# Kernel optimization log

Hardware: AMD Instinct MI355X
Metric: run time of the kernel (lower is better)

The kernel has to match this reference:

```python
import jax, jax.numpy as jnp
import numpy as np

B = 4096
L = 15          # self.length
NINP = 256      # emb_size
NHID = 512      # hidden_size
VOCAB = 30005
TOPK = 10
K = 4 * TOPK + 2   # 42 actions
N_SPLIT = 2 * TOPK
N_STEP = 5      # num_edits
PAD = 30003


def _lstm_dir(x, Wih, Whh, b, reverse):
    # x: [T,B,D]; Wih: [4H,D]; Whh: [4H,H]; b: [4H] (b_ih+b_hh). PyTorch gate order i,f,g,o.
    Bsz, H = x.shape[1], Whh.shape[1]
    def step(carry, xt):
        h, c = carry
        z = xt @ Wih.T + h @ Whh.T + b
        i, f, g, o = jnp.split(z, 4, axis=-1)
        c = jax.nn.sigmoid(f) * c + jax.nn.sigmoid(i) * jnp.tanh(g)
        h = jax.nn.sigmoid(o) * jnp.tanh(c)
        return (h, c), h
    h0 = jnp.zeros((Bsz, H), x.dtype)
    _, ys = jax.lax.scan(step, (h0, h0), x, reverse=reverse)
    return ys  # [T,B,H], position-aligned for both directions


def bilstm(x, Wih0, Whh0, b0, Wih1, Whh1, b1):
    # x: [B,T,D] -> [B,T,2H]; 2-layer bidirectional, zero initial state (matches c0/h0 zeros).
    xt = jnp.swapaxes(x, 0, 1)
    for Wih, Whh, b in ((Wih0, Whh0, b0), (Wih1, Whh1, b1)):
        fw = _lstm_dir(xt, Wih[0], Whh[0], b[0], False)
        bw = _lstm_dir(xt, Wih[1], Whh[1], b[1], True)
        xt = jnp.concatenate([fw, bw], axis=-1)
    return jnp.swapaxes(xt, 0, 1)


def policy_step(st_1, length_t, pos, emb0, key_pos, rep_words, valid_id,
                emb_table, enc_table, Wih0, Whh0, b0, Wih1, Whh1, b1,
                del_vec, hold_vec, mlp_W, mlp_b, mlp1_W, mlp1_b):
    Bsz = st_1.shape[0]
    pos_row = jnp.zeros((L,), jnp.float32).at[pos].set(1.0)         # static pos
    pos_tensor = jnp.broadcast_to(pos_row[None, :, None], (Bsz, L, 1))
    embt = emb_table[st_1] * (1.0 - pos_tensor)
    x = jnp.concatenate([embt, emb0, pos_tensor], axis=2)            # [B,L,2*ninp+1]
    out = bilstm(x, Wih0, Whh0, b0, Wih1, Whh1, b1)                  # [B,L,2*nhid]
    pooled = out[:, pos, :]
    representation = jnp.concatenate(
        [pooled, key_pos[:, pos:pos + 1], jnp.broadcast_to(pos_row[None, :], (Bsz, L))], axis=1)
    # external encoder output is detached in the original
    word_emb = jax.lax.stop_gradient(enc_table[rep_words])           # [B,4*topk,ninp]
    emb2 = jnp.concatenate([word_emb,
                            jnp.broadcast_to(del_vec, (Bsz, 1, NINP)),
                            jnp.broadcast_to(hold_vec, (Bsz, 1, NINP))], axis=1)  # [B,K,ninp]
    onehot = jnp.broadcast_to(jnp.eye(K, dtype=jnp.float32)[None], (Bsz, K, K))
    emb2 = jnp.concatenate([emb2, onehot], axis=2)                   # [B,K,ninp+K]
    rep100 = representation @ mlp_W.T + mlp_b                        # [B,100]
    emb100 = emb2 @ mlp1_W.T + mlp1_b                                # [B,K,100]
    score = jnp.einsum('bkd,bd->bk', emb100, rep100)
    policy = jax.nn.softmax(score, axis=1)
    action = jnp.argmax(policy, axis=1, keepdims=True).astype(jnp.int32)  # eval mode
    pi = jnp.take_along_axis(policy, action, axis=1)                 # [B,1]

    rep_b = (action < N_SPLIT).astype(jnp.int32)
    replaceflag = rep_b * valid_id
    ins_b = ((action >= N_SPLIT) & (action < 2 * N_SPLIT)).astype(jnp.int32)
    insertflag = ins_b * valid_id * (length_t + ins_b <= 15).astype(jnp.int32)
    del_b = (action == 2 * N_SPLIT).astype(jnp.int32)
    deleteflag = del_b * valid_id * (length_t - del_b > 2).astype(jnp.int32)
    holdflag = 1 - replaceflag - insertflag - deleteflag

    action_words = jnp.take_along_axis(rep_words, jnp.clip(action, 0, N_SPLIT - 1), axis=1)  # [B,1]
    rep_seq = jnp.concatenate([action_words, st_1[:, pos + 1:]], axis=1)
    ins_seq = jnp.concatenate([action_words, st_1[:, pos:-1]], axis=1)
    padding = jnp.full((Bsz, 1), PAD, dtype=st_1.dtype)
    del_seq = jnp.concatenate([st_1[:, pos + 1:], padding], axis=1)
    hol_seq = st_1[:, pos:]
    new_tail = (rep_seq * replaceflag + ins_seq * insertflag
                + del_seq * deleteflag + hol_seq * holdflag)
    st = st_1.at[:, pos:].set(new_tail)
    length_tt = insertflag + length_t - deleteflag
    return st, pi, action.astype(jnp.float32), length_tt


def setup_inputs() -> dict:
    key = jax.random.key(0)
    ks = jax.random.split(key, 20)
    s = 0.05
    in0 = 2 * NINP + 1
    in1 = 2 * NHID
    inp = {
        'input_ids': jax.random.randint(ks[0], (B, L), 0, 30000, dtype=jnp.int32),
        'key_pos': jax.random.uniform(ks[1], (B, L), dtype=jnp.float32),
        'sequence_length': jax.random.randint(ks[2], (B, 1), 3, 16, dtype=jnp.int32),
        'rep_words_all': jax.random.randint(ks[3], (B, N_STEP, 4 * TOPK), 0, 30000, dtype=jnp.int32),
        'valid_id_all': jax.random.randint(ks[4], (B, N_STEP, 1), 0, 2, dtype=jnp.int32),
        'emb_table': jax.random.normal(ks[5], (VOCAB, NINP), jnp.float32) * s,
        'enc_table': jax.random.normal(ks[6], (VOCAB, NINP), jnp.float32) * s,
        'Wih0': jax.random.normal(ks[7], (2, 4 * NHID, in0), jnp.float32) * s,
        'Whh0': jax.random.normal(ks[8], (2, 4 * NHID, NHID), jnp.float32) * s,
        'b0': jax.random.normal(ks[9], (2, 4 * NHID), jnp.float32) * s,
        'Wih1': jax.random.normal(ks[10], (2, 4 * NHID, in1), jnp.float32) * s,
        'Whh1': jax.random.normal(ks[11], (2, 4 * NHID, NHID), jnp.float32) * s,
        'b1': jax.random.normal(ks[12], (2, 4 * NHID), jnp.float32) * s,
        'del_vec': jax.random.uniform(ks[13], (1, 1, NINP), dtype=jnp.float32),
        'hold_vec': jax.random.uniform(ks[14], (1, 1, NINP), dtype=jnp.float32),
        'mlp_W': jax.random.normal(ks[15], (100, 2 * NHID + 1 + L), jnp.float32) * s,
        'mlp_b': jnp.zeros((100,), jnp.float32),
        'mlp1_W': jax.random.normal(ks[16], (100, NINP + K), jnp.float32) * s,
        'mlp1_b': jnp.zeros((100,), jnp.float32),
    }
    return inp


def reference(input_ids, key_pos, sequence_length, rep_words_all, valid_id_all,
              emb_table, enc_table, Wih0, Whh0, b0, Wih1, Whh1, b1,
              del_vec, hold_vec, mlp_W, mlp_b, mlp1_W, mlp1_b):
    st = input_ids
    emb0 = emb_table[input_ids]            # embedding of s0, computed once
    length_t = sequence_length
    pis, acts = [], []
    for i in range(N_STEP):
        pos = i % (L - 3) + 2              # static per unrolled step
        st, pi, a, length_t = policy_step(
            st, length_t, pos, emb0, key_pos,
            rep_words_all[:, i, :], valid_id_all[:, i, :],
            emb_table, enc_table, Wih0, Whh0, b0, Wih1, Whh1, b1,
            del_vec, hold_vec, mlp_W, mlp_b, mlp1_W, mlp1_b)
        pis.append(pi)
        acts.append(a)
    pis = jnp.concatenate(pis, axis=1)     # [B,N_STEP]
    actions = jnp.concatenate(acts, axis=1)
    return pis, actions, st, length_t
```

## Files before the change

kernel.cpp:

```cpp
#include <hip/hip_runtime.h>

#define B_ 4096
#define L_ 15
#define NSTEP_ 5
#define VOC_ 30005
#define PAD_ 30003

typedef _Float16 f16;
typedef f16  f16x8 __attribute__((ext_vector_type(8)));
typedef float f32x16 __attribute__((ext_vector_type(16)));

__device__ __forceinline__ float sigf(float x){ return 1.0f/(1.0f+expf(-x)); }

#define MFMA_(d,a,b) d = __builtin_amdgcn_mfma_f32_32x32x16_f16(a,b,d,0,0,0)

struct RecParams {
  const f16 *A1h_0,*A1l_0,*A1h_1,*A1l_1;
  const f16 *A2h_0,*A2l_0,*A2h_1,*A2l_1;
  const f16 *Wfh_0,*Wfl_0,*Wfh_1,*Wfl_1;
  const float *bias_0,*bias_1;
  const f16 *embH,*embL;
  const int *st,*ids;
  float *c_0,*c_1,*h2_0,*h2_1;
  f16 *hh_0,*hl_0,*hh_1,*hl_1;
  int lda1, lda2, ldh, ldh2, k1p, k2p, first, gather, t_0, t_1, pos, b0c, act0, act1;
};

__device__ __forceinline__ int swz(int row, int s){
  int u = ((row&7)<<1) | s;
  return ((row>>3)<<8) + ((u ^ (u>>1))<<4);
}

__global__ __launch_bounds__(256,2) void rec_gemm(RecParams p){
  const int bxe = blockIdx.x;
  const int ct4 = bxe & 15;
  const int dir = bxe >> 4;
  if (!(dir ? p.act1 : p.act0)) return;
  const f16* A1h = dir ? p.A1h_1 : p.A1h_0;
  const f16* A1l = dir ? p.A1l_1 : p.A1l_0;
  const f16* A2h = dir ? p.A2h_1 : p.A2h_0;
  const f16* A2l = dir ? p.A2l_1 : p.A2l_0;
  const f16* Wfh = dir ? p.Wfh_1 : p.Wfh_0;
  const f16* Wfl = dir ? p.Wfl_1 : p.Wfl_0;
  const float* bias = dir ? p.bias_1 : p.bias_0;
  float* cbuf = dir ? p.c_1 : p.c_0;
  float* h2   = dir ? p.h2_1 : p.h2_0;
  f16* hhb = dir ? p.hh_1 : p.hh_0;
  f16* hlb = dir ? p.hl_1 : p.hl_0;
  const int tcur = dir ? p.t_1 : p.t_0;

  const int tid  = threadIdx.x;
  const int lane = tid & 63;
  const int w    = tid >> 6;
  const int mbase = blockIdx.y*128;

  __shared__ union {
    float z[128*128];
    f16   stg[8][2048];
  } sm;

  f32x16 accM[2][2], accX[2][2];
#pragma unroll
  for (int i=0;i<2;i++)
#pragma unroll
    for (int j=0;j<2;j++)
#pragma unroll
      for (int r=0;r<16;r++){ accM[i][j][r]=0.f; accX[i][j][r]=0.f; }

  const int arow = (w&1)*64 + (lane&31);
  const int fs = lane>>5;
  const int aoff0 = swz(arow,    fs), aoff1 = swz(arow+32, fs);

  const int ct0 = ct4*4 + (w>>1)*2;
  const f16* WfhL = Wfh + (size_t)lane*8;
  const f16* WflL = Wfl + (size_t)lane*8;

  const int srow = tid >> 1, ss = tid & 1;
  const int sws = swz(srow, ss);
  const int ktot = p.k1p + p.k2p;

  int tokT=0, tokI=0, zflag=0;
  if (p.gather){
    int gb = p.b0c + mbase + srow;
    tokT = p.st [gb*L_ + tcur];
    tokI = p.ids[gb*L_ + tcur];
    zflag = (tcur == p.pos) ? 1 : 0;
  }

  f16x8 ra_h0, ra_l0, ra_h1, ra_l1;
  const f16x8 zero8 = {0,0,0,0,0,0,0,0};

  auto gload = [&](int ph){
    if (ph >= ktot) return;
    if (ph < p.k1p){
      if (p.gather){
        if (ph < 8){
          if (zflag){ ra_h0=zero8; ra_l0=zero8; ra_h1=zero8; ra_l1=zero8; }
          else {
            size_t base = (size_t)tokT*256 + ph*32 + ss*8;
            ra_h0 = *(const f16x8*)(p.embH + base);
            ra_l0 = *(const f16x8*)(p.embL + base);
            ra_h1 = *(const f16x8*)(p.embH + base + 16);
            ra_l1 = *(const f16x8*)(p.embL + base + 16);
          }
        } else if (ph < 16){
          size_t base = (size_t)tokI*256 + (ph-8)*32 + ss*8;
          ra_h0 = *(const f16x8*)(p.embH + base);
          ra_l0 = *(const f16x8*)(p.embL + base);
          ra_h1 = *(const f16x8*)(p.embH + base + 16);
          ra_l1 = *(const f16x8*)(p.embL + base + 16);
        } else {
          ra_h0 = zero8; ra_l0 = zero8; ra_h1 = zero8; ra_l1 = zero8;
          if (ss == 0) ra_h0[0] = zflag ? (f16)1.0f : (f16)0.0f;
        }
      } else {
        long base = (long)(mbase+srow)*p.lda1 + ph*32 + ss*8;
        ra_h0 = *(const f16x8*)(A1h + base);
        ra_l0 = *(const f16x8*)(A1l + base);
        ra_h1 = *(const f16x8*)(A1h + base + 16);
        ra_l1 = *(const f16x8*)(A1l + base + 16);
      }
    } else {
      long base = (long)(mbase+srow)*p.lda2 + (ph - p.k1p)*32 + ss*8;
      ra_h0 = *(const f16x8*)(A2h + base);
      ra_l0 = *(const f16x8*)(A2l + base);
      ra_h1 = *(const f16x8*)(A2h + base + 16);
      ra_l1 = *(const f16x8*)(A2l + base + 16);
    }
  };
  auto swrite = [&](int buf){
    *(f16x8*)((char*)sm.stg[buf*4+0] + sws) = ra_h0;
    *(f16x8*)((char*)sm.stg[buf*4+1] + sws) = ra_l0;
    *(f16x8*)((char*)sm.stg[buf*4+2] + sws) = ra_h1;
    *(f16x8*)((char*)sm.stg[buf*4+3] + sws) = ra_l1;
  };
  auto loadB = [&](int ph, f16x8* rb){
    size_t base0 = ((size_t)(ph*2+0)*64 + ct0)*512;
    size_t base1 = ((size_t)(ph*2+1)*64 + ct0)*512;
    rb[0] = *(const f16x8*)(WfhL + base0);
    rb[1] = *(const f16x8*)(WfhL + base0 + 512);
    rb[2] = *(const f16x8*)(WflL + base0);
    rb[3] = *(const f16x8*)(WflL + base0 + 512);
    rb[4] = *(const f16x8*)(WfhL + base1);
    rb[5] = *(const f16x8*)(WfhL + base1 + 512);
    rb[6] = *(const f16x8*)(WflL + base1);
    rb[7] = *(const f16x8*)(WflL + base1 + 512);
  };

  gload(0); swrite(0); gload(1);
  f16x8 rb[8];
  loadB(0, rb);
  asm volatile("s_waitcnt lgkmcnt(0)" ::: "memory");
  __builtin_amdgcn_s_barrier();

  for (int ph=0; ph<ktot; ++ph){
    const int cur = ph & 1;
    const char* s0h = (const char*)sm.stg[cur*4+0];
    const char* s0l = (const char*)sm.stg[cur*4+1];
    const char* s1h = (const char*)sm.stg[cur*4+2];
    const char* s1l = (const char*)sm.stg[cur*4+3];
    f16x8 a00h = *(const f16x8*)(s0h + aoff0);
    f16x8 a01h = *(const f16x8*)(s0h + aoff1);
    f16x8 a00l = *(const f16x8*)(s0l + aoff0);
    f16x8 a01l = *(const f16x8*)(s0l + aoff1);
    f16x8 a10h = *(const f16x8*)(s1h + aoff0);
    f16x8 a11h = *(const f16x8*)(s1h + aoff1);
    f16x8 a10l = *(const f16x8*)(s1l + aoff0);
    f16x8 a11l = *(const f16x8*)(s1l + aoff1);
    if (ph+1 < ktot){ swrite((ph+1)&1); gload(ph+2); }
    MFMA_(accM[0][0], a00h, rb[0]); MFMA_(accX[0][0], a00h, rb[2]); MFMA_(accX[0][0], a00l, rb[0]);
    MFMA_(accM[1][0], a01h, rb[0]); MFMA_(accX[1][0], a01h, rb[2]); MFMA_(accX[1][0], a01l, rb[0]);
    MFMA_(accM[0][1], a00h, rb[1]); MFMA_(accX[0][1], a00h, rb[3]); MFMA_(accX[0][1], a00l, rb[1]);
    MFMA_(accM[1][1], a01h, rb[1]); MFMA_(accX[1][1], a01h, rb[3]); MFMA_(accX[1][1], a01l, rb[1]);
    MFMA_(accM[0][0], a10h, rb[4]); MFMA_(accX[0][0], a10h, rb[6]); MFMA_(accX[0][0], a10l, rb[4]);
    MFMA_(accM[1][0], a11h, rb[4]); MFMA_(accX[1][0], a11h, rb[6]); MFMA_(accX[1][0], a11l, rb[4]);
    MFMA_(accM[0][1], a10h, rb[5]); MFMA_(accX[0][1], a10h, rb[7]); MFMA_(accX[0][1], a10l, rb[5]);
    MFMA_(accM[1][1], a11h, rb[5]); MFMA_(accX[1][1], a11h, rb[7]); MFMA_(accX[1][1], a11l, rb[5]);
    if (ph+1 < ktot) loadB(ph+1, rb);
    asm volatile("s_waitcnt lgkmcnt(0)" ::: "memory");
    __builtin_amdgcn_s_barrier();
  }

#pragma unroll
  for (int tm=0;tm<2;tm++)
#pragma unroll
   for (int tn=0;tn<2;tn++){
    int lcol = (w>>1)*64 + tn*32 + (lane&31);
    float bv = bias[ct4*128 + lcol];
#pragma unroll
    for (int r=0;r<16;r++){
      int lrow = (w&1)*64 + tm*32 + (r&3) + 8*(r>>2) + 4*(lane>>5);
      sm.z[lrow*128 + lcol] = accM[tm][tn][r] + 0.000244140625f*accX[tm][tn][r] + bv;
    }
   }
  __syncthreads();

  const int nb = ct4*32;
#pragma unroll
  for (int it=0; it<16; ++it){
    int idx = it*256 + tid;
    int nq = idx & 31, row = idx >> 5;
    float4 g4 = *(const float4*)&sm.z[row*128 + nq*4];
    int m = mbase + row, n = nb + nq;
    float cp = p.first ? 0.f : cbuf[(size_t)m*512 + n];
    float cc = sigf(g4.y)*cp + sigf(g4.x)*tanhf(g4.z);
    float hv = sigf(g4.w)*tanhf(cc);
    cbuf[(size_t)m*512 + n] = cc;
    f16 hi = (f16)hv;
    f16 lo = (f16)((hv - (float)hi)*4096.0f);
    hhb[(size_t)m*p.ldh + n] = hi;
    hlb[(size_t)m*p.ldh + n] = lo;
    if (h2) h2[(size_t)m*p.ldh2 + n] = hv;
  }
}

__global__ void prep_w0(const float* Wih, const float* Whh, const float* b0,
                        f16* Wfh, f16* Wfl, float* bp){
  int gid = blockIdx.x*blockDim.x + threadIdx.x;
  const int PER_DIR = 66*64*64*8;
  if (gid >= 2*PER_DIR) return;
  int dir = gid / PER_DIR;
  int rem = gid % PER_DIR;
  int j = rem & 7, lane = (rem>>3)&63, ct = (rem>>9)&63, kt16 = rem>>15;
  int n4g = ct*32 + (lane&31);
  int n = n4g>>2, g = n4g&3;
  int srow = dir*2048 + g*512 + n;
  int k = kt16*16 + ((lane>>5)<<3) + j;
  float v;
  if (k < 513)       v = Wih[(size_t)srow*513 + k];
  else if (k < 544)  v = 0.f;
  else               v = Whh[(size_t)srow*512 + (k-544)];
  f16 hi = (f16)v;
  Wfh[gid] = hi;
  Wfl[gid] = (f16)((v - (float)hi)*4096.0f);
  if (kt16==0 && (lane>>5)==0 && j==0) bp[dir*2048 + n4g] = b0[srow];
}

__global__ void prep_w1(const float* Wih, const float* Whh, const float* b1,
                        f16* Wfh, f16* Wfl, float* bp){
  int gid = blockIdx.x*blockDim.x + threadIdx.x;
  const int PER_DIR = 96*64*64*8;
  if (gid >= 2*PER_DIR) return;
  int dir = gid / PER_DIR;
  int rem = gid % PER_DIR;
  int j = rem & 7, lane = (rem>>3)&63, ct = (rem>>9)&63, kt16 = rem>>15;
  int n4g = ct*32 + (lane&31);
  int n = n4g>>2, g = n4g&3;
  int srow = dir*2048 + g*512 + n;
  int k = kt16*16 + ((lane>>5)<<3) + j;
  float v;
  if (k < 1024) v = Wih[(size_t)srow*1024 + k];
  else          v = Whh[(size_t)srow*512 + (k-1024)];
  f16 hi = (f16)v;
  Wfh[gid] = hi;
  Wfl[gid] = (f16)((v - (float)hi)*4096.0f);
  if (kt16==0 && (lane>>5)==0 && j==0) bp[dir*2048 + n4g] = b1[srow];
}

__global__ void prep_emb(const float* emb, f16* eh, f16* el){
  int gid = blockIdx.x*blockDim.x + threadIdx.x;
  if (gid >= VOC_*256) return;
  float v = emb[gid];
  f16 hi = (f16)v;
  eh[gid] = hi;
  el[gid] = (f16)((v - (float)hi)*4096.0f);
}

__global__ void prep_mlpwt(const float* mW, float* wt){
  int gid = blockIdx.x*blockDim.x + threadIdx.x;
  if (gid >= 100*1040) return;
  int j = gid / 1040, k = gid % 1040;
  wt[k*100 + j] = mW[gid];
}

__global__ __launch_bounds__(128) void prep_encproj(const float* enc, const float* delv,
                        const float* holdv, const float* m1W, const float* m1b, float* ep){
  int r = blockIdx.x;
  __shared__ float row[256];
  const float* src = (r < VOC_) ? enc + (size_t)r*256 : (r == VOC_ ? delv : holdv);
  for (int i=threadIdx.x;i<256;i+=128) row[i]=src[i];
  __syncthreads();
  int j = threadIdx.x;
  if (j < 100){
    double s = (double)m1b[j];
    const float* wr = m1W + (size_t)j*298;
    for (int k=0;k<256;k++) s += (double)wr[k] * (double)row[k];
    ep[(size_t)r*100 + j] = (float)s;
  }
}

__global__ void init_st(const int* ids, const int* seqlen, int* st, int* len){
  int gid = blockIdx.x*blockDim.x + threadIdx.x;
  if (gid < B_*L_) st[gid] = ids[gid];
  if (gid < B_)    len[gid] = seqlen[gid];
}

__global__ void sentinel(float* out, float v){
  int gid = blockIdx.x*blockDim.x + threadIdx.x;
  if (gid < B_*NSTEP_) out[gid] = v;
}

__global__ __launch_bounds__(128) void score_update(
    const float* pooled, const float* keypos, const float* mWt, const float* mb,
    const float* ep, const float* m1W, const int* repw, const int* valid,
    int* st, int* len, float* outPis, float* outActs, int step, int pos, int b0){
  int b = blockIdx.x;
  int bg = b0 + b;
  __shared__ float rep[1040];
  __shared__ float r100[100];
  __shared__ double sc[42];
  int tid = threadIdx.x;
  for (int i=tid;i<1024;i+=128) rep[i] = pooled[(size_t)b*1024+i];
  if (tid < 16){
    if (tid == 0) rep[1024] = keypos[bg*L_+pos];
    else          rep[1024+tid] = ((tid-1)==pos) ? 1.f : 0.f;
  }
  __syncthreads();
  if (tid < 100){
    double s = (double)mb[tid];
    for (int k=0;k<1040;k++) s += (double)mWt[k*100+tid] * (double)rep[k];
    r100[tid] = (float)s;
  }
  __syncthreads();
  if (tid < 42){
    int row = (tid < 40) ? repw[((size_t)bg*NSTEP_+step)*40 + tid] : (VOC_ + (tid-40));
    const float* er = ep + (size_t)row*100;
    double s = 0.0;
    for (int j=0;j<100;j++) s += (double)er[j] * (double)r100[j];
    for (int j=0;j<100;j++) s += (double)m1W[j*298 + 256 + tid] * (double)r100[j];
    sc[tid] = s;
  }
  __syncthreads();
  if (tid == 0){
    double mx = sc[0]; int am = 0;
    for (int k=1;k<42;k++) if (sc[k] > mx){ mx = sc[k]; am = k; }
    double sum = 0.0;
    for (int k=0;k<42;k++) sum += exp(sc[k]-mx);
    float pi = (float)(1.0/sum);
    int vid = valid[bg*NSTEP_+step];
    int ln  = len[bg];
    int repb = (am < 20) ? 1 : 0;
    int insb = (am >= 20 && am < 40) ? 1 : 0;
    int delb = (am == 40) ? 1 : 0;
    int repf = repb*vid;
    int insf = insb*vid*(((ln+insb) <= 15) ? 1 : 0);
    int delf = delb*vid*(((ln-delb) >  2) ? 1 : 0);
    int T = L_ - pos;
    int tail[13];
    for (int j=0;j<T;j++) tail[j] = st[bg*L_+pos+j];
    int aw = repw[((size_t)bg*NSTEP_+step)*40 + (am < 20 ? am : 19)];
    for (int j=0;j<T;j++){
      int rv = (j==0) ? aw : tail[j];
      int iv = (j==0) ? aw : tail[j-1];
      int dv = (j < T-1) ? tail[j+1] : PAD_;
      int hv = tail[j];
      int nv = repf ? rv : (insf ? iv : (delf ? dv : hv));
      st[bg*L_+pos+j] = nv;
    }
    len[bg] = ln + insf - delf;
    outPis[bg*NSTEP_+step]  = pi;
    outActs[bg*NSTEP_+step] = (float)am;
  }
}

__global__ void finalize(const int* st, const int* len, float* out){
  int gid = blockIdx.x*blockDim.x + threadIdx.x;
  if (gid < B_*L_)            out[2*B_*NSTEP_ + gid] = (float)st[gid];
  else if (gid < B_*L_ + B_)  out[2*B_*NSTEP_ + B_*L_ + (gid - B_*L_)] = (float)len[gid - B_*L_];
}

extern "C" void kernel_launch(void* const* d_in, const int* in_sizes, int n_in,
                              void* d_out, int out_size, void* d_ws, size_t ws_size,
                              hipStream_t stream) {
  const int*   ids    = (const int*)  d_in[0];
  const float* keypos = (const float*)d_in[1];
  const int*   seqlen = (const int*)  d_in[2];
  const int*   repw   = (const int*)  d_in[3];
  const int*   valid  = (const int*)  d_in[4];
  const float* emb    = (const float*)d_in[5];
  const float* enc    = (const float*)d_in[6];
  const float* Wih0   = (const float*)d_in[7];
  const float* Whh0   = (const float*)d_in[8];
  const float* b0     = (const float*)d_in[9];
  const float* Wih1   = (const float*)d_in[10];
  const float* Whh1   = (const float*)d_in[11];
  const float* b1     = (const float*)d_in[12];
  const float* delv   = (const float*)d_in[13];
  const float* holdv  = (const float*)d_in[14];
  const float* mW     = (const float*)d_in[15];
  const float* mb     = (const float*)d_in[16];
  const float* m1W    = (const float*)d_in[17];
  const float* m1b    = (const float*)d_in[18];
  float* out = (float*)d_out;

  const int NKW0 = 66, NKW1 = 96;
  const size_t W0PD = (size_t)NKW0*64*64*8;
  const size_t W1PD = (size_t)NKW1*64*64*8;

  char* ws = (char*)d_ws;
  size_t off = 0;
  auto allocB = [&](size_t bytes) -> char* {
    char* pp = ws + off; off += (bytes + 255) & ~size_t(255); return pp;
  };
  f16*  Wf0h = (f16*)allocB(2*W0PD*2);
  f16*  Wf0l = (f16*)allocB(2*W0PD*2);
  f16*  Wf1h = (f16*)allocB(2*W1PD*2);
  f16*  Wf1l = (f16*)allocB(2*W1PD*2);
  float* bp0 = (float*)allocB(4096*4);
  float* bp1 = (float*)allocB(4096*4);
  f16*  embH = (f16*)allocB((size_t)VOC_*256*2);
  f16*  embL = (f16*)allocB((size_t)VOC_*256*2);
  float* mWt = (float*)allocB(104000*4);
  float* ep  = (float*)allocB((size_t)30007*100*4);
  int* stbuf  = (int*)allocB(B_*L_*4);
  int* lenbuf = (int*)allocB(B_*4);
  size_t fixedB = off;

  const int cands[6] = {4096, 2048, 1024, 512, 256, 128};
  int Bc = 0;
  for (int ci=0; ci<6; ++ci){
    size_t c = cands[ci];
    size_t chunkB = c*(size_t)(15*1024*2*2 + 4*512*2*2 + 2*512*4 + 2*512*4 + 1024*4) + 8*256;
    if (fixedB + chunkB <= ws_size){ Bc = (int)c; break; }
  }
  if (!Bc){
    float code = 100000.0f + (float)(ws_size >> 20);
    sentinel<<<(B_*NSTEP_+255)/256,256,0,stream>>>(out, code);
    return;
  }
  f16* o0h = (f16*)allocB((size_t)L_*Bc*1024*2);
  f16* o0l = (f16*)allocB((size_t)L_*Bc*1024*2);
  f16* h1h = (f16*)allocB((size_t)4*Bc*512*2);
  f16* h1l = (f16*)allocB((size_t)4*Bc*512*2);
  float* c0 = (float*)allocB((size_t)2*Bc*512*4);
  float* c1 = (float*)allocB((size_t)2*Bc*512*4);
  float* pooled = (float*)allocB((size_t)Bc*1024*4);

  prep_w0<<<(int)((2*W0PD+255)/256),256,0,stream>>>(Wih0, Whh0, b0, Wf0h, Wf0l, bp0);
  prep_w1<<<(int)((2*W1PD+255)/256),256,0,stream>>>(Wih1, Whh1, b1, Wf1h, Wf1l, bp1);
  prep_emb<<<(VOC_*256+255)/256,256,0,stream>>>(emb, embH, embL);
  prep_mlpwt<<<(100*1040+255)/256,256,0,stream>>>(mW, mWt);
  prep_encproj<<<30007,128,0,stream>>>(enc, delv, holdv, m1W, m1b, ep);
  init_st<<<(B_*L_+255)/256,256,0,stream>>>(ids, seqlen, stbuf, lenbuf);

  for (int b0c=0; b0c<B_; b0c+=Bc){
    for (int step=0; step<NSTEP_; ++step){
      int pos = step + 2;

      for (int ts=0; ts<L_; ++ts){
        int tf = ts, tb = 14-ts;
        RecParams p{};
        p.gather = 1; p.t_0 = tf; p.t_1 = tb; p.pos = pos; p.b0c = b0c;
        p.embH = embH; p.embL = embL; p.st = stbuf; p.ids = ids;
        p.k1p = 17; p.k2p = ts ? 16 : 0;
        size_t of0 = (size_t)(ts?tf-1:0)*Bc*1024;
        size_t of1 = (size_t)(ts?tb+1:0)*Bc*1024 + (ts?512:0);
        p.A2h_0 = o0h + of0;  p.A2l_0 = o0l + of0;
        p.A2h_1 = o0h + of1;  p.A2l_1 = o0l + of1;
        p.lda2 = 1024;
        p.Wfh_0 = Wf0h;        p.Wfl_0 = Wf0l;
        p.Wfh_1 = Wf0h + W0PD; p.Wfl_1 = Wf0l + W0PD;
        p.bias_0 = bp0; p.bias_1 = bp0 + 2048;
        p.c_0 = c0; p.c_1 = c0 + (size_t)Bc*512;
        p.hh_0 = o0h + (size_t)tf*Bc*1024;       p.hl_0 = o0l + (size_t)tf*Bc*1024;
        p.hh_1 = o0h + (size_t)tb*Bc*1024 + 512; p.hl_1 = o0l + (size_t)tb*Bc*1024 + 512;
        p.ldh = 1024;
        p.h2_0 = nullptr; p.h2_1 = nullptr; p.ldh2 = 1024;
        p.first = (ts==0); p.act0 = 1; p.act1 = 1;
        rec_gemm<<<dim3(32,Bc/128),256,0,stream>>>(p);
      }

      int nL1 = L_ - pos;
      for (int ts=0; ts<nL1; ++ts){
        RecParams p{};
        int tf = ts, tb = 14-ts;
        int parR = (ts-1)&1, parW = ts&1;
        p.gather = 0;
        p.A1h_0 = o0h + (size_t)tf*Bc*1024;  p.A1l_0 = o0l + (size_t)tf*Bc*1024;
        p.A1h_1 = o0h + (size_t)tb*Bc*1024;  p.A1l_1 = o0l + (size_t)tb*Bc*1024;
        p.lda1 = 1024; p.k1p = 32;
        p.k2p  = ts ? 16 : 0;
        size_t r0 = (size_t)(0*2 + (ts?parR:0))*Bc*512;
        size_t r1 = (size_t)(1*2 + (ts?parR:0))*Bc*512;
        p.A2h_0 = h1h + r0; p.A2l_0 = h1l + r0;
        p.A2h_1 = h1h + r1; p.A2l_1 = h1l + r1;
        p.lda2 = 512;
        p.Wfh_0 = Wf1h;        p.Wfl_0 = Wf1l;
        p.Wfh_1 = Wf1h + W1PD; p.Wfl_1 = Wf1l + W1PD;
        p.bias_0 = bp1; p.bias_1 = bp1 + 2048;
        p.c_0 = c1; p.c_1 = c1 + (size_t)Bc*512;
        size_t w0 = (size_t)(0*2 + parW)*Bc*512;
        size_t w1 = (size_t)(1*2 + parW)*Bc*512;
        p.hh_0 = h1h + w0; p.hl_0 = h1l + w0;
        p.hh_1 = h1h + w1; p.hl_1 = h1l + w1;
        p.ldh = 512;
        p.h2_0 = (ts == pos)    ? pooled        : nullptr;
        p.h2_1 = (ts == 14-pos) ? (pooled+512)  : nullptr;
        p.ldh2 = 1024;
        p.first = (ts==0);
        p.act0 = (ts <= pos) ? 1 : 0; p.act1 = 1;
        rec_gemm<<<dim3(32,Bc/128),256,0,stream>>>(p);
      }

      score_update<<<Bc,128,0,stream>>>(pooled, keypos, mWt, mb, ep, m1W, repw, valid,
                                        stbuf, lenbuf, out, out + B_*NSTEP_, step, pos, b0c);
    }
  }
  finalize<<<(B_*L_+B_+255)/256,256,0,stream>>>(stbuf, lenbuf, out);
}
```

Baseline: 21.43 ms.

## Stage A tiles via direct global-to-LDS loads with a triple-buffered pipeline

The recurrent GEMM kernel now copies A-operand tiles straight from global memory into LDS with global_load_lds, instead of loading them into registers and then writing LDS. The staging buffer grows from double to triple buffering with a two-phase lookahead, and waits use vmcnt. B-fragment loads are split in half so the second half overlaps the first half's MFMAs, and s_setprio raises priority around the MFMA block. Constant zero/one flag rows are kept in a small global buffer so the gather path can also use direct LDS loads, at the cost of more LDS and more fragile wait-count tuning.

```diff
diff --git a/kernel.cpp b/kernel.cpp
--- a/kernel.cpp
+++ b/kernel.cpp
@@ -14,12 +14,18 @@
 
 #define MFMA_(d,a,b) d = __builtin_amdgcn_mfma_f32_32x32x16_f16(a,b,d,0,0,0)
 
+__device__ __forceinline__ void gll16(const f16* g, f16* l){
+  __builtin_amdgcn_global_load_lds(
+      (const __attribute__((address_space(1))) void*)g,
+      (__attribute__((address_space(3))) void*)l, 16, 0, 0);
+}
+
 struct RecParams {
   const f16 *A1h_0,*A1l_0,*A1h_1,*A1l_1;
   const f16 *A2h_0,*A2l_0,*A2h_1,*A2l_1;
   const f16 *Wfh_0,*Wfl_0,*Wfh_1,*Wfl_1;
   const float *bias_0,*bias_1;
-  const f16 *embH,*embL;
+  const f16 *embH,*embL,*flagpg;
   const int *st,*ids;
   float *c_0,*c_1,*h2_0,*h2_1;
   f16 *hh_0,*hl_0,*hh_1,*hl_1;
@@ -56,7 +62,7 @@
 
   __shared__ union {
     float z[128*128];
-    f16   stg[8][2048];
+    f16   stg[3][4][2048];
   } sm;
 
   f32x16 accM[2][2], accX[2][2];
@@ -75,90 +81,75 @@
   const f16* WfhL = Wfh + (size_t)lane*8;
   const f16* WflL = Wfl + (size_t)lane*8;
 
-  const int srow = tid >> 1, ss = tid & 1;
-  const int sws = swz(srow, ss);
+  int ug = tid & 15; ug ^= ug>>1; ug ^= ug>>2;
+  const int rowS = ((tid>>4)<<3) + (ug>>1);
+  const int sS   = ug & 1;
   const int ktot = p.k1p + p.k2p;
 
   int tokT=0, tokI=0, zflag=0;
   if (p.gather){
-    int gb = p.b0c + mbase + srow;
+    int gb = p.b0c + mbase + rowS;
     tokT = p.st [gb*L_ + tcur];
     tokI = p.ids[gb*L_ + tcur];
     zflag = (tcur == p.pos) ? 1 : 0;
   }
-
-  f16x8 ra_h0, ra_l0, ra_h1, ra_l1;
-  const f16x8 zero8 = {0,0,0,0,0,0,0,0};
-
-  auto gload = [&](int ph){
-    if (ph >= ktot) return;
+  const f16* zeros = p.flagpg + 8;
+  const f16* ones0 = p.flagpg;
+
+  auto stage = [&](int ph, int buf){
+    f16* d0 = &sm.stg[buf][0][w<<9];
+    f16* d1 = &sm.stg[buf][1][w<<9];
+    f16* d2 = &sm.stg[buf][2][w<<9];
+    f16* d3 = &sm.stg[buf][3][w<<9];
     if (ph < p.k1p){
       if (p.gather){
         if (ph < 8){
-          if (zflag){ ra_h0=zero8; ra_l0=zero8; ra_h1=zero8; ra_l1=zero8; }
+          if (zflag){ gll16(zeros,d0); gll16(zeros,d1); gll16(zeros,d2); gll16(zeros,d3); }
           else {
-            size_t base = (size_t)tokT*256 + ph*32 + ss*8;
-            ra_h0 = *(const f16x8*)(p.embH + base);
-            ra_l0 = *(const f16x8*)(p.embL + base);
-            ra_h1 = *(const f16x8*)(p.embH + base + 16);
-            ra_l1 = *(const f16x8*)(p.embL + base + 16);
+            size_t base = (size_t)tokT*256 + ph*32 + sS*8;
+            gll16(p.embH+base, d0); gll16(p.embL+base, d1);
+            gll16(p.embH+base+16, d2); gll16(p.embL+base+16, d3);
           }
         } else if (ph < 16){
-          size_t base = (size_t)tokI*256 + (ph-8)*32 + ss*8;
-          ra_h0 = *(const f16x8*)(p.embH + base);
-          ra_l0 = *(const f16x8*)(p.embL + base);
-          ra_h1 = *(const f16x8*)(p.embH + base + 16);
-          ra_l1 = *(const f16x8*)(p.embL + base + 16);
+          size_t base = (size_t)tokI*256 + (ph-8)*32 + sS*8;
+          gll16(p.embH+base, d0); gll16(p.embL+base, d1);
+          gll16(p.embH+base+16, d2); gll16(p.embL+base+16, d3);
         } else {
-          ra_h0 = zero8; ra_l0 = zero8; ra_h1 = zero8; ra_l1 = zero8;
-          if (ss == 0) ra_h0[0] = zflag ? (f16)1.0f : (f16)0.0f;
+          const f16* s0 = (sS==0 && zflag) ? ones0 : zeros;
+          gll16(s0,d0); gll16(zeros,d1); gll16(zeros,d2); gll16(zeros,d3);
         }
       } else {
-        long base = (long)(mbase+srow)*p.lda1 + ph*32 + ss*8;
-        ra_h0 = *(const f16x8*)(A1h + base);
-        ra_l0 = *(const f16x8*)(A1l + base);
-        ra_h1 = *(const f16x8*)(A1h + base + 16);
-        ra_l1 = *(const f16x8*)(A1l + base + 16);
+        long base = (long)(mbase+rowS)*p.lda1 + ph*32 + sS*8;
+        gll16(A1h+base, d0); gll16(A1l+base, d1);
+        gll16(A1h+base+16, d2); gll16(A1l+base+16, d3);
       }
     } else {
-      long base = (long)(mbase+srow)*p.lda2 + (ph - p.k1p)*32 + ss*8;
-      ra_h0 = *(const f16x8*)(A2h + base);
-      ra_l0 = *(const f16x8*)(A2l + base);
-      ra_h1 = *(const f16x8*)(A2h + base + 16);
-      ra_l1 = *(const f16x8*)(A2l + base + 16);
+      long base = (long)(mbase+rowS)*p.lda2 + (ph - p.k1p)*32 + sS*8;
+      gll16(A2h+base, d0); gll16(A2l+base, d1);
+      gll16(A2h+base+16, d2); gll16(A2l+base+16, d3);
     }
   };
-  auto swrite = [&](int buf){
-    *(f16x8*)((char*)sm.stg[buf*4+0] + sws) = ra_h0;
-    *(f16x8*)((char*)sm.stg[buf*4+1] + sws) = ra_l0;
-    *(f16x8*)((char*)sm.stg[buf*4+2] + sws) = ra_h1;
-    *(f16x8*)((char*)sm.stg[buf*4+3] + sws) = ra_l1;
+  auto loadB = [&](int kt16, f16x8* r){
+    size_t base = ((size_t)kt16*64 + ct0)*512;
+    r[0] = *(const f16x8*)(WfhL + base);
+    r[1] = *(const f16x8*)(WfhL + base + 512);
+    r[2] = *(const f16x8*)(WflL + base);
+    r[3] = *(const f16x8*)(WflL + base + 512);
   };
-  auto loadB = [&](int ph, f16x8* rb){
-    size_t base0 = ((size_t)(ph*2+0)*64 + ct0)*512;
-    size_t base1 = ((size_t)(ph*2+1)*64 + ct0)*512;
-    rb[0] = *(const f16x8*)(WfhL + base0);
-    rb[1] = *(const f16x8*)(WfhL + base0 + 512);
-    rb[2] = *(const f16x8*)(WflL + base0);
-    rb[3] = *(const f16x8*)(WflL + base0 + 512);
-    rb[4] = *(const f16x8*)(WfhL + base1);
-    rb[5] = *(const f16x8*)(WfhL + base1 + 512);
-    rb[6] = *(const f16x8*)(WflL + base1);
-    rb[7] = *(const f16x8*)(WflL + base1 + 512);
-  };
-
-  gload(0); swrite(0); gload(1);
-  f16x8 rb[8];
-  loadB(0, rb);
-  asm volatile("s_waitcnt lgkmcnt(0)" ::: "memory");
+
+  f16x8 rb0[4], rb1[4];
+  stage(0,0); stage(1,1);
+  loadB(0, rb0);
+  asm volatile("s_waitcnt vmcnt(8)" ::: "memory");
   __builtin_amdgcn_s_barrier();
-
+  __builtin_amdgcn_sched_barrier(0);
+
+  int bR = 0;
   for (int ph=0; ph<ktot; ++ph){
-    const int cur = ph & 1;
-    const char* s0h = (const char*)sm.stg[cur*4+0];
-    const char* s0l = (const char*)sm.stg[cur*4+1];
-    const char* s1h = (const char*)sm.stg[cur*4+2];
-    const char* s1l = (const char*)sm.stg[cur*4+3];
+    const char* s0h = (const char*)sm.stg[bR][0];
+    const char* s0l = (const char*)sm.stg[bR][1];
+    const char* s1h = (const char*)sm.stg[bR][2];
+    const char* s1l = (const char*)sm.stg[bR][3];
     f16x8 a00h = *(const f16x8*)(s0h + aoff0);
     f16x8 a01h = *(const f16x8*)(s0h + aoff1);
     f16x8 a00l = *(const f16x8*)(s0l + aoff0);
@@ -167,19 +158,26 @@
     f16x8 a11h = *(const f16x8*)(s1h + aoff1);
     f16x8 a10l = *(const f16x8*)(s1l + aoff0);
     f16x8 a11l = *(const f16x8*)(s1l + aoff1);
-    if (ph+1 < ktot){ swrite((ph+1)&1); gload(ph+2); }
-    MFMA_(accM[0][0], a00h, rb[0]); MFMA_(accX[0][0], a00h, rb[2]); MFMA_(accX[0][0], a00l, rb[0]);
-    MFMA_(accM[1][0], a01h, rb[0]); MFMA_(accX[1][0], a01h, rb[2]); MFMA_(accX[1][0], a01l, rb[0]);
-    MFMA_(accM[0][1], a00h, rb[1]); MFMA_(accX[0][1], a00h, rb[3]); MFMA_(accX[0][1], a00l, rb[1]);
-    MFMA_(accM[1][1], a01h, rb[1]); MFMA_(accX[1][1], a01h, rb[3]); MFMA_(accX[1][1], a01l, rb[1]);
-    MFMA_(accM[0][0], a10h, rb[4]); MFMA_(accX[0][0], a10h, rb[6]); MFMA_(accX[0][0], a10l, rb[4]);
-    MFMA_(accM[1][0], a11h, rb[4]); MFMA_(accX[1][0], a11h, rb[6]); MFMA_(accX[1][0], a11l, rb[4]);
-    MFMA_(accM[0][1], a10h, rb[5]); MFMA_(accX[0][1], a10h, rb[7]); MFMA_(accX[0][1], a10l, rb[5]);
-    MFMA_(accM[1][1], a11h, rb[5]); MFMA_(accX[1][1], a11h, rb[7]); MFMA_(accX[1][1], a11l, rb[5]);
-    if (ph+1 < ktot) loadB(ph+1, rb);
-    asm volatile("s_waitcnt lgkmcnt(0)" ::: "memory");
+    loadB(2*ph+1, rb1);
+    if (ph+2 < ktot) stage(ph+2, (bR+2>=3)?(bR-1):(bR+2));
+    __builtin_amdgcn_s_setprio(1);
+    MFMA_(accM[0][0], a00h, rb0[0]); MFMA_(accX[0][0], a00h, rb0[2]); MFMA_(accX[0][0], a00l, rb0[0]);
+    MFMA_(accM[1][0], a01h, rb0[0]); MFMA_(accX[1][0], a01h, rb0[2]); MFMA_(accX[1][0], a01l, rb0[0]);
+    MFMA_(accM[0][1], a00h, rb0[1]); MFMA_(accX[0][1], a00h, rb0[3]); MFMA_(accX[0][1], a00l, rb0[1]);
+    MFMA_(accM[1][1], a01h, rb0[1]); MFMA_(accX[1][1], a01h, rb0[3]); MFMA_(accX[1][1], a01l, rb0[1]);
+    MFMA_(accM[0][0], a10h, rb1[0]); MFMA_(accX[0][0], a10h, rb1[2]); MFMA_(accX[0][0], a10l, rb1[0]);
+    MFMA_(accM[1][0], a11h, rb1[0]); MFMA_(accX[1][0], a11h, rb1[2]); MFMA_(accX[1][0], a11l, rb1[0]);
+    MFMA_(accM[0][1], a10h, rb1[1]); MFMA_(accX[0][1], a10h, rb1[3]); MFMA_(accX[0][1], a10l, rb1[1]);
+    MFMA_(accM[1][1], a11h, rb1[1]); MFMA_(accX[1][1], a11h, rb1[3]); MFMA_(accX[1][1], a11l, rb1[1]);
+    __builtin_amdgcn_s_setprio(0);
+    if (ph+1 < ktot) loadB(2*ph+2, rb0);
+    asm volatile("s_waitcnt vmcnt(8) lgkmcnt(0)" ::: "memory");
     __builtin_amdgcn_s_barrier();
-  }
+    __builtin_amdgcn_sched_barrier(0);
+    bR = (bR+1==3)?0:(bR+1);
+  }
+
+  __syncthreads();
 
 #pragma unroll
   for (int tm=0;tm<2;tm++)
@@ -289,10 +287,11 @@
   }
 }
 
-__global__ void init_st(const int* ids, const int* seqlen, int* st, int* len){
+__global__ void init_st(const int* ids, const int* seqlen, int* st, int* len, f16* flagpg){
   int gid = blockIdx.x*blockDim.x + threadIdx.x;
   if (gid < B_*L_) st[gid] = ids[gid];
   if (gid < B_)    len[gid] = seqlen[gid];
+  if (gid < 16)    flagpg[gid] = (gid==0) ? (f16)1.0f : (f16)0.0f;
 }
 
 __global__ void sentinel(float* out, float v){
@@ -393,9 +392,8 @@
   const float* m1b    = (const float*)d_in[18];
   float* out = (float*)d_out;
 
-  const int NKW0 = 66, NKW1 = 96;
-  const size_t W0PD = (size_t)NKW0*64*64*8;
-  const size_t W1PD = (size_t)NKW1*64*64*8;
+  const size_t W0PD = (size_t)66*64*64*8;
+  const size_t W1PD = (size_t)96*64*64*8;
 
   char* ws = (char*)d_ws;
   size_t off = 0;
@@ -414,6 +412,7 @@
   float* ep  = (float*)allocB((size_t)30007*100*4);
   int* stbuf  = (int*)allocB(B_*L_*4);
   int* lenbuf = (int*)allocB(B_*4);
+  f16* flagpg = (f16*)allocB(256);
   size_t fixedB = off;
 
   const int cands[6] = {4096, 2048, 1024, 512, 256, 128};
@@ -441,7 +440,7 @@
   prep_emb<<<(VOC_*256+255)/256,256,0,stream>>>(emb, embH, embL);
   prep_mlpwt<<<(100*1040+255)/256,256,0,stream>>>(mW, mWt);
   prep_encproj<<<30007,128,0,stream>>>(enc, delv, holdv, m1W, m1b, ep);
-  init_st<<<(B_*L_+255)/256,256,0,stream>>>(ids, seqlen, stbuf, lenbuf);
+  init_st<<<(B_*L_+255)/256,256,0,stream>>>(ids, seqlen, stbuf, lenbuf, flagpg);
 
   for (int b0c=0; b0c<B_; b0c+=Bc){
     for (int step=0; step<NSTEP_; ++step){
@@ -451,7 +450,7 @@
         int tf = ts, tb = 14-ts;
         RecParams p{};
         p.gather = 1; p.t_0 = tf; p.t_1 = tb; p.pos = pos; p.b0c = b0c;
-        p.embH = embH; p.embL = embL; p.st = stbuf; p.ids = ids;
+        p.embH = embH; p.embL = embL; p.flagpg = flagpg; p.st = stbuf; p.ids = ids;
         p.k1p = 17; p.k2p = ts ? 16 : 0;
         size_t of0 = (size_t)(ts?tf-1:0)*Bc*1024;
         size_t of1 = (size_t)(ts?tb+1:0)*Bc*1024 + (ts?512:0);
@@ -475,7 +474,7 @@
         RecParams p{};
         int tf = ts, tb = 14-ts;
         int parR = (ts-1)&1, parW = ts&1;
-        p.gather = 0;
+        p.gather = 0; p.flagpg = flagpg;
         p.A1h_0 = o0h + (size_t)tf*Bc*1024;  p.A1l_0 = o0l + (size_t)tf*Bc*1024;
         p.A1h_1 = o0h + (size_t)tb*Bc*1024;  p.A1l_1 = o0l + (size_t)tb*Bc*1024;
         p.lda1 = 1024; p.k1p = 32;
```

Measured after the change: 21.90 ms. 1.02x slower.
